# Performance work log

Hardware: AMD Instinct MI355X
Metric: run time of the kernel (lower is better)

## Reference

```python
import jax, jax.numpy as jnp
import numpy as np

MARGIN = 0.4
ALPHA = 0.01


def _pairwise_dist(emb):
    sq = jnp.sum(emb * emb, axis=1)
    d2 = jnp.maximum(sq[:, None] + sq[None, :] - 2.0 * (emb @ emb.T), 0.0)
    safe = jnp.where(d2 > 0, d2, 1.0)
    return jnp.where(d2 > 0, jnp.sqrt(safe), 0.0)


def setup_inputs() -> dict:
    key = jax.random.key(0)
    ka, kp, kn = jax.random.split(key, 3)
    B, D = 4096, 128
    return {
        "a": jax.random.normal(ka, (B, D), dtype=jnp.float32),
        "p": jax.random.normal(kp, (B, D), dtype=jnp.float32),
        "n": jax.random.normal(kn, (B, D), dtype=jnp.float32),
    }


def reference(a, p, n):
    B = a.shape[0]
    emb = jnp.concatenate([a, p, n], axis=0)            # [3B, D]
    labels = jnp.tile(jnp.arange(B), 3)                 # [3B]
    dist = _pairwise_dist(emb)                          # [3B, 3B]
    same = labels[:, None] == labels[None, :]           # exactly 3 True per row (incl. diag)
    # Every row has >=2 positives (3 incl. self) and >=1 negative, so all rows count.
    pos_max = jnp.max(jnp.where(same, dist, -jnp.inf), axis=1)
    neg_min = jnp.min(jnp.where(same, jnp.inf, dist), axis=1)
    loss = jnp.mean(jnp.maximum(pos_max - neg_min + MARGIN, 0.0))
    reg = jnp.mean((jnp.abs(emb) - 1.0) ** 2)
    return loss + ALPHA * reg
```

## Files before the change

### kernel.cpp

```cpp
#include <hip/hip_runtime.h>

#define NROWS 12288
#define BSZ   4096
#define DIM   128
#define CSPLIT 16
#define COLS_PER_BLOCK (NROWS / CSPLIT)
#define NSTRIPS (COLS_PER_BLOCK / 32)

typedef __bf16 bf16x8 __attribute__((ext_vector_type(8)));
typedef float  f32x4  __attribute__((ext_vector_type(4)));

__device__ __forceinline__ unsigned short f2bf(float f) {
  unsigned int u = __float_as_uint(f);
  u = u + 0x7FFFu + ((u >> 16) & 1u);
  return (unsigned short)(u >> 16);
}
__device__ __forceinline__ float bf2f(unsigned short h) {
  return __uint_as_float(((unsigned int)h) << 16);
}

__global__ void prep_k(const float* __restrict__ a, const float* __restrict__ p,
                       const float* __restrict__ nn,
                       unsigned short* __restrict__ embh, float* __restrict__ sq,
                       unsigned int* __restrict__ negbits,
                       float* __restrict__ posmax2, float* __restrict__ regpart) {
  const int w = threadIdx.x >> 6, lane = threadIdx.x & 63;
  const int i = blockIdx.x * 4 + w;
  const float2 av = reinterpret_cast<const float2*>(a  + (size_t)i * DIM)[lane];
  const float2 pv = reinterpret_cast<const float2*>(p  + (size_t)i * DIM)[lane];
  const float2 nv = reinterpret_cast<const float2*>(nn + (size_t)i * DIM)[lane];

  const unsigned short ha0 = f2bf(av.x), ha1 = f2bf(av.y);
  const unsigned short hp0 = f2bf(pv.x), hp1 = f2bf(pv.y);
  const unsigned short hn0 = f2bf(nv.x), hn1 = f2bf(nv.y);
  reinterpret_cast<ushort2*>(embh + (size_t)i * DIM)[lane]             = make_ushort2(ha0, ha1);
  reinterpret_cast<ushort2*>(embh + (size_t)(BSZ + i) * DIM)[lane]     = make_ushort2(hp0, hp1);
  reinterpret_cast<ushort2*>(embh + (size_t)(2 * BSZ + i) * DIM)[lane] = make_ushort2(hn0, hn1);

  float rax = bf2f(ha0), ray = bf2f(ha1);
  float rpx = bf2f(hp0), rpy = bf2f(hp1);
  float rnx = bf2f(hn0), rny = bf2f(hn1);
  float sa = rax * rax + ray * ray;
  float sp = rpx * rpx + rpy * rpy;
  float sn = rnx * rnx + rny * rny;

  float t0 = fabsf(av.x) - 1.f, t1 = fabsf(av.y) - 1.f;
  float t2 = fabsf(pv.x) - 1.f, t3 = fabsf(pv.y) - 1.f;
  float t4 = fabsf(nv.x) - 1.f, t5 = fabsf(nv.y) - 1.f;
  float rg = t0 * t0 + t1 * t1 + t2 * t2 + t3 * t3 + t4 * t4 + t5 * t5;

  float dx, dy;
  dx = av.x - pv.x; dy = av.y - pv.y; float dap = dx * dx + dy * dy;
  dx = av.x - nv.x; dy = av.y - nv.y; float dan = dx * dx + dy * dy;
  dx = pv.x - nv.x; dy = pv.y - nv.y; float dpn = dx * dx + dy * dy;

  for (int m = 32; m; m >>= 1) {
    sa  += __shfl_xor(sa, m);  sp  += __shfl_xor(sp, m);  sn  += __shfl_xor(sn, m);
    rg  += __shfl_xor(rg, m);
    dap += __shfl_xor(dap, m); dan += __shfl_xor(dan, m); dpn += __shfl_xor(dpn, m);
  }
  if (lane == 0) {
    sq[i] = sa; sq[BSZ + i] = sp; sq[2 * BSZ + i] = sn;
    negbits[i] = negbits[BSZ + i] = negbits[2 * BSZ + i] = 0x7F800000u;
    posmax2[i]           = fmaxf(dap, dan);
    posmax2[BSZ + i]     = fmaxf(dap, dpn);
    posmax2[2 * BSZ + i] = fmaxf(dan, dpn);
    regpart[i] = rg;
  }
}

__global__ __launch_bounds__(256, 3) void negmin_k(
    const unsigned short* __restrict__ embh,
    const float* __restrict__ sq,
    unsigned int* __restrict__ negbits) {
  __shared__ __align__(16) char ldsB[2][8192];
  const int tid  = threadIdx.x;
  const int w    = tid >> 6;
  const int lane = tid & 63;
  const int c16  = lane & 15;
  const int q    = lane >> 4;
  const int wRow    = blockIdx.x * 256 + w * 64;
  const int colBase = blockIdx.y * COLS_PER_BLOCK;
  const int rot     = blockIdx.x % NSTRIPS;

  bf16x8 afrag[4][4];
  {
    const char* abase = (const char*)embh + (size_t)(wRow + c16) * 256 + q * 16;
#pragma unroll
    for (int mt = 0; mt < 4; ++mt)
#pragma unroll
      for (int ks = 0; ks < 4; ++ks)
        afrag[mt][ks] = *reinterpret_cast<const bf16x8*>(abase + mt * 4096 + ks * 64);
  }

  float minv[4][4];
#pragma unroll
  for (int mt = 0; mt < 4; ++mt)
#pragma unroll
    for (int r = 0; r < 4; ++r) minv[mt][r] = __builtin_inff();

  auto stage = [&](int sidx, int b) {
#pragma unroll
    for (int h = 0; h < 2; ++h) {
      const int kc = w * 2 + h;
      const char* gp = (const char*)embh +
          (size_t)(colBase + sidx * 32 + (kc & 1) * 16 + c16) * 256 +
          (kc >> 1) * 64 + q * 16;
      __builtin_amdgcn_global_load_lds(
          (const __attribute__((address_space(1))) unsigned int*)gp,
          (__attribute__((address_space(3))) unsigned int*)(&ldsB[b][kc * 1024]),
          16, 0, 0);
    }
  };

  int strip = rot;
  stage(strip, 0);
  __syncthreads();
  {
    int s1 = strip + 1; if (s1 >= NSTRIPS) s1 -= NSTRIPS;
    stage(s1, 1);
  }

  for (int c = 0; c < NSTRIPS; ++c) {
    const int b = c & 1;
    const int colStart = colBase + strip * 32;
    const float sq0 = sq[colStart + c16];
    const float sq1 = sq[colStart + 16 + c16];

    f32x4 acc[4][2] = {};
#pragma unroll
    for (int ks = 0; ks < 4; ++ks)
#pragma unroll
      for (int ct = 0; ct < 2; ++ct) {
        const bf16x8 bfr =
            *reinterpret_cast<const bf16x8*>(&ldsB[b][(ks * 2 + ct) * 1024 + lane * 16]);
#pragma unroll
        for (int mt = 0; mt < 4; ++mt)
          acc[mt][ct] =
              __builtin_amdgcn_mfma_f32_16x16x32_bf16(afrag[mt][ks], bfr, acc[mt][ct], 0, 0, 0);
      }

    __syncthreads();
    if (c + 2 < NSTRIPS) {
      int s2 = strip + 2; if (s2 >= NSTRIPS) s2 -= NSTRIPS;
      stage(s2, b);
    }

    const int dd = (colStart - wRow) & 4095;
    if (dd < 76 || dd > 4064) {
#pragma unroll
      for (int mt = 0; mt < 4; ++mt)
#pragma unroll
        for (int ct = 0; ct < 2; ++ct) {
          const float sqb = ct ? sq1 : sq0;
          const int lvc = dd + ct * 16 + c16 - q * 4;
#pragma unroll
          for (int r = 0; r < 4; ++r) {
            float v = fmaf(-2.f, acc[mt][ct][r], sqb);
            const int K = mt * 16 + r;
            if (lvc == K || lvc == K + 4096) v = __builtin_inff();
            minv[mt][r] = fminf(minv[mt][r], v);
          }
        }
    } else {
#pragma unroll
      for (int mt = 0; mt < 4; ++mt)
#pragma unroll
        for (int ct = 0; ct < 2; ++ct) {
          const float sqb = ct ? sq1 : sq0;
#pragma unroll
          for (int r = 0; r < 4; ++r)
            minv[mt][r] = fminf(minv[mt][r], fmaf(-2.f, acc[mt][ct][r], sqb));
        }
    }

    strip = strip + 1; if (strip >= NSTRIPS) strip -= NSTRIPS;
  }

#pragma unroll
  for (int mt = 0; mt < 4; ++mt)
#pragma unroll
    for (int r = 0; r < 4; ++r) {
      float v = minv[mt][r];
      v = fminf(v, __shfl_xor(v, 1));
      v = fminf(v, __shfl_xor(v, 2));
      v = fminf(v, __shfl_xor(v, 4));
      v = fminf(v, __shfl_xor(v, 8));
      if (c16 == 0) {
        const int row = wRow + mt * 16 + q * 4 + r;
        float d2 = sq[row] + v;
        d2 = fmaxf(d2, 0.f);
        atomicMin(&negbits[row], __float_as_uint(d2));
      }
    }
}

__global__ void final_k(const float* __restrict__ posmax2,
                        const unsigned int* __restrict__ negbits,
                        const float* __restrict__ regpart, float* __restrict__ out) {
  __shared__ float red[16], redr[16];
  const int tid = threadIdx.x;
  float s = 0.f;
  for (int i = tid; i < NROWS; i += 1024) {
    const float pm = sqrtf(posmax2[i]);
    const float nm = sqrtf(__uint_as_float(negbits[i]));
    s += fmaxf(pm - nm + 0.4f, 0.f);
  }
  float rg = 0.f;
  for (int i = tid; i < BSZ; i += 1024) rg += regpart[i];
  for (int m = 32; m; m >>= 1) { s += __shfl_xor(s, m); rg += __shfl_xor(rg, m); }
  if ((tid & 63) == 0) { red[tid >> 6] = s; redr[tid >> 6] = rg; }
  __syncthreads();
  if (tid == 0) {
    float t = 0.f, tr = 0.f;
#pragma unroll
    for (int k = 0; k < 16; ++k) { t += red[k]; tr += redr[k]; }
    out[0] = t / (float)NROWS + 0.01f * (tr / (float)(NROWS * DIM));
  }
}

extern "C" void kernel_launch(void* const* d_in, const int* in_sizes, int n_in,
                              void* d_out, int out_size, void* d_ws, size_t ws_size,
                              hipStream_t stream) {
  const float* a  = (const float*)d_in[0];
  const float* p  = (const float*)d_in[1];
  const float* nn = (const float*)d_in[2];
  float* out = (float*)d_out;
  char* ws = (char*)d_ws;

  const size_t EMBH_BYTES = (size_t)NROWS * DIM * 2;
  unsigned short* embh    = (unsigned short*)ws;
  float*          sq      = (float*)(ws + EMBH_BYTES);
  unsigned int*   negbit  = (unsigned int*)(ws + EMBH_BYTES + (size_t)NROWS * 4);
  float*          pos2    = (float*)(ws + EMBH_BYTES + (size_t)NROWS * 8);
  float*          regpart = (float*)(ws + EMBH_BYTES + (size_t)NROWS * 12);

  prep_k<<<BSZ / 4, 256, 0, stream>>>(a, p, nn, embh, sq, negbit, pos2, regpart);
  negmin_k<<<dim3(NROWS / 256, CSPLIT), 256, 0, stream>>>(embh, sq, negbit);
  final_k<<<1, 1024, 0, stream>>>(pos2, negbit, regpart, out);
}
```

Before: 112.5 us.

## Triple-buffer LDS B tiles with register prefetch and fuse final reduction via last-block

```diff
diff --git a/kernel.cpp b/kernel.cpp
--- a/kernel.cpp
+++ b/kernel.cpp
@@ -6,6 +6,8 @@
 #define CSPLIT 16
 #define COLS_PER_BLOCK (NROWS / CSPLIT)
 #define NSTRIPS (COLS_PER_BLOCK / 32)
+#define GRIDX (NROWS / 256)
+#define TOTAL_BLOCKS (GRIDX * CSPLIT)
 
 typedef __bf16 bf16x8 __attribute__((ext_vector_type(8)));
 typedef float  f32x4  __attribute__((ext_vector_type(4)));
@@ -23,7 +25,9 @@
                        const float* __restrict__ nn,
                        unsigned short* __restrict__ embh, float* __restrict__ sq,
                        unsigned int* __restrict__ negbits,
-                       float* __restrict__ posmax2, float* __restrict__ regpart) {
+                       float* __restrict__ posmax2, float* __restrict__ regpart,
+                       unsigned int* __restrict__ done) {
+  if (blockIdx.x == 0 && threadIdx.x == 0) *done = 0u;
   const int w = threadIdx.x >> 6, lane = threadIdx.x & 63;
   const int i = blockIdx.x * 4 + w;
   const float2 av = reinterpret_cast<const float2*>(a  + (size_t)i * DIM)[lane];
@@ -72,8 +76,14 @@
 __global__ __launch_bounds__(256, 3) void negmin_k(
     const unsigned short* __restrict__ embh,
     const float* __restrict__ sq,
-    unsigned int* __restrict__ negbits) {
-  __shared__ __align__(16) char ldsB[2][8192];
+    unsigned int* __restrict__ negbits,
+    const float* __restrict__ posmax2,
+    const float* __restrict__ regpart,
+    unsigned int* __restrict__ done,
+    float* __restrict__ out) {
+  __shared__ __align__(16) char ldsB[3][8192];
+  __shared__ float red[4], redr[4];
+  __shared__ int lastFlag;
   const int tid  = threadIdx.x;
   const int w    = tid >> 6;
   const int lane = tid & 63;
@@ -115,14 +125,25 @@
 
   int strip = rot;
   stage(strip, 0);
+  { int s1 = strip + 1; if (s1 >= NSTRIPS) s1 -= NSTRIPS; stage(s1, 1); }
   __syncthreads();
-  {
-    int s1 = strip + 1; if (s1 >= NSTRIPS) s1 -= NSTRIPS;
-    stage(s1, 1);
-  }
+
+  bf16x8 bfr[8], bfrN[8];
+#pragma unroll
+  for (int f = 0; f < 8; ++f)
+    bfr[f] = *reinterpret_cast<const bf16x8*>(&ldsB[0][f * 1024 + lane * 16]);
 
   for (int c = 0; c < NSTRIPS; ++c) {
-    const int b = c & 1;
+    if (c + 2 < NSTRIPS) {
+      int s2 = strip + 2; if (s2 >= NSTRIPS) s2 -= NSTRIPS;
+      stage(s2, (c + 2) % 3);
+    }
+    if (c + 1 < NSTRIPS) {
+      const char* nb = ldsB[(c + 1) % 3];
+#pragma unroll
+      for (int f = 0; f < 8; ++f)
+        bfrN[f] = *reinterpret_cast<const bf16x8*>(nb + f * 1024 + lane * 16);
+    }
     const int colStart = colBase + strip * 32;
     const float sq0 = sq[colStart + c16];
     const float sq1 = sq[colStart + 16 + c16];
@@ -132,19 +153,14 @@
     for (int ks = 0; ks < 4; ++ks)
 #pragma unroll
       for (int ct = 0; ct < 2; ++ct) {
-        const bf16x8 bfr =
-            *reinterpret_cast<const bf16x8*>(&ldsB[b][(ks * 2 + ct) * 1024 + lane * 16]);
+        const bf16x8 bb = bfr[ks * 2 + ct];
 #pragma unroll
         for (int mt = 0; mt < 4; ++mt)
           acc[mt][ct] =
-              __builtin_amdgcn_mfma_f32_16x16x32_bf16(afrag[mt][ks], bfr, acc[mt][ct], 0, 0, 0);
+              __builtin_amdgcn_mfma_f32_16x16x32_bf16(afrag[mt][ks], bb, acc[mt][ct], 0, 0, 0);
       }
 
     __syncthreads();
-    if (c + 2 < NSTRIPS) {
-      int s2 = strip + 2; if (s2 >= NSTRIPS) s2 -= NSTRIPS;
-      stage(s2, b);
-    }
 
     const int dd = (colStart - wRow) & 4095;
     if (dd < 76 || dd > 4064) {
@@ -174,6 +190,8 @@
         }
     }
 
+#pragma unroll
+    for (int f = 0; f < 8; ++f) bfr[f] = bfrN[f];
     strip = strip + 1; if (strip >= NSTRIPS) strip -= NSTRIPS;
   }
 
@@ -193,29 +211,30 @@
         atomicMin(&negbits[row], __float_as_uint(d2));
       }
     }
-}
-
-__global__ void final_k(const float* __restrict__ posmax2,
-                        const unsigned int* __restrict__ negbits,
-                        const float* __restrict__ regpart, float* __restrict__ out) {
-  __shared__ float red[16], redr[16];
-  const int tid = threadIdx.x;
-  float s = 0.f;
-  for (int i = tid; i < NROWS; i += 1024) {
-    const float pm = sqrtf(posmax2[i]);
-    const float nm = sqrtf(__uint_as_float(negbits[i]));
-    s += fmaxf(pm - nm + 0.4f, 0.f);
-  }
-  float rg = 0.f;
-  for (int i = tid; i < BSZ; i += 1024) rg += regpart[i];
-  for (int m = 32; m; m >>= 1) { s += __shfl_xor(s, m); rg += __shfl_xor(rg, m); }
-  if ((tid & 63) == 0) { red[tid >> 6] = s; redr[tid >> 6] = rg; }
+
   __syncthreads();
   if (tid == 0) {
-    float t = 0.f, tr = 0.f;
-#pragma unroll
-    for (int k = 0; k < 16; ++k) { t += red[k]; tr += redr[k]; }
-    out[0] = t / (float)NROWS + 0.01f * (tr / (float)(NROWS * DIM));
+    __threadfence();
+    const unsigned int prev = atomicAdd(done, 1u);
+    lastFlag = (prev == TOTAL_BLOCKS - 1) ? 1 : 0;
+  }
+  __syncthreads();
+  if (lastFlag) {
+    float s = 0.f, rg = 0.f;
+    for (int i = tid; i < NROWS; i += 256) {
+      const float pm = sqrtf(posmax2[i]);
+      const unsigned int nb = atomicMin(&negbits[i], 0x7F800000u);
+      s += fmaxf(pm - sqrtf(__uint_as_float(nb)) + 0.4f, 0.f);
+    }
+    for (int i = tid; i < BSZ; i += 256) rg += regpart[i];
+    for (int m = 32; m; m >>= 1) { s += __shfl_xor(s, m); rg += __shfl_xor(rg, m); }
+    if (lane == 0) { red[w] = s; redr[w] = rg; }
+    __syncthreads();
+    if (tid == 0) {
+      const float t  = red[0] + red[1] + red[2] + red[3];
+      const float tr = redr[0] + redr[1] + redr[2] + redr[3];
+      out[0] = t / (float)NROWS + 0.01f * (tr / (float)(NROWS * DIM));
+    }
   }
 }
 
@@ -234,8 +253,8 @@
   unsigned int*   negbit  = (unsigned int*)(ws + EMBH_BYTES + (size_t)NROWS * 4);
   float*          pos2    = (float*)(ws + EMBH_BYTES + (size_t)NROWS * 8);
   float*          regpart = (float*)(ws + EMBH_BYTES + (size_t)NROWS * 12);
-
-  prep_k<<<BSZ / 4, 256, 0, stream>>>(a, p, nn, embh, sq, negbit, pos2, regpart);
-  negmin_k<<<dim3(NROWS / 256, CSPLIT), 256, 0, stream>>>(embh, sq, negbit);
-  final_k<<<1, 1024, 0, stream>>>(pos2, negbit, regpart, out);
-}
+  unsigned int*   done    = (unsigned int*)(ws + EMBH_BYTES + (size_t)NROWS * 12 + (size_t)BSZ * 4);
+
+  prep_k<<<BSZ / 4, 256, 0, stream>>>(a, p, nn, embh, sq, negbit, pos2, regpart, done);
+  negmin_k<<<dim3(GRIDX, CSPLIT), 256, 0, stream>>>(embh, sq, negbit, pos2, regpart, done, out);
+}
```

Measured after the change: 157.6 us. +40.2%, slower.
